# Performance work log

Hardware: AMD Instinct MI355X
Metric: run time of the kernel (lower is better)

Reference implementation:

```python
import jax, jax.numpy as jnp
import numpy as np


def _conv1x1(x, w, b):
    # x:[B,C,H,W], w:[O,C,1,1], b:[O]
    y = jax.lax.conv_general_dilated(x, w, (1, 1), 'SAME',
                                     dimension_numbers=('NCHW', 'OIHW', 'NCHW'))
    return y + b[None, :, None, None]


def _dwconv3x3(x, w, b):
    # depthwise: x:[B,C,H,W2], w:[C,1,3,3], b:[C]
    c = x.shape[1]
    y = jax.lax.conv_general_dilated(x, w, (1, 1), 'SAME',
                                     dimension_numbers=('NCHW', 'OIHW', 'NCHW'),
                                     feature_group_count=c)
    return y + b[None, :, None, None]


def setup_inputs() -> dict:
    key = jax.random.key(0)
    k1, k2, k3, k4, k5 = jax.random.split(key, 5)
    B, C, H, W = 4, 64, 256, 256
    x = jax.random.normal(k1, (B, C, H, W), dtype=jnp.float32)
    # qkv 1x1 conv params: [3C, C, 1, 1]
    w_qkv = jax.random.normal(k2, (3 * C, C, 1, 1), dtype=jnp.float32) * (1.0 / np.sqrt(C))
    b_qkv = jax.random.normal(k3, (3 * C,), dtype=jnp.float32) * 0.01
    # depthwise 3x3 conv params: [C, 1, 3, 3]
    w_dw = jax.random.normal(k4, (C, 1, 3, 3), dtype=jnp.float32) * (1.0 / 3.0)
    b_dw = jax.random.normal(k5, (C,), dtype=jnp.float32) * 0.01
    return {"x": x, "w_qkv": w_qkv, "b_qkv": b_qkv, "w_dw": w_dw, "b_dw": b_dw}


def reference(x, w_qkv, b_qkv, w_dw, b_dw):
    # qkv projection and split into q, k, v  (each [B,C,H,W])
    qkv = _conv1x1(x, w_qkv, b_qkv)
    q, k, v = jnp.split(qkv, 3, axis=1)
    # per-channel spatial attention scores: q @ k^T over last dim -> [B,C,H,H]
    scores = jnp.einsum('bchw,bcgw->bchg', q, k)
    # depthwise 3x3 conv on the [H,H] score map, then softmax over last dim
    attn = jax.nn.softmax(_dwconv3x3(scores, w_dw, b_dw), axis=-1)
    # attn @ v + residual -> [B,C,H,W]
    return jnp.einsum('bchg,bcgw->bchw', attn, v) + x
```

## Files before the change

### kernel.cpp

```cpp
#include <hip/hip_runtime.h>
#include <math.h>

#define B 4
#define C 64
#define H 256
#define W 256
#define HW (H*W)
#define CHW (C*HW)
#define BCHW (B*CHW)

typedef _Float16 half8v __attribute__((ext_vector_type(8)));
typedef float f32x4 __attribute__((ext_vector_type(4)));


__device__ inline ushort f16_bits(float f) {
    _Float16 h = (_Float16)f;
    return *(ushort*)&h;
}

__global__ __launch_bounds__(256, 4) void qkv_kernel(
    const float* __restrict__ x, const float* __restrict__ w,
    const float* __restrict__ bias, ushort* __restrict__ qkv)
{
    __shared__ ushort tile[48 * 264];
    int t = threadIdx.x;
    int lane = t & 63, wv = t >> 6;
    int l15 = lane & 15, l4 = lane >> 4;
    int p0 = blockIdx.x * 256;
    int b = p0 >> 16;
    int ppx = p0 & (HW - 1);
    int pxw = ppx + wv * 64;

    const float* xb = x + (size_t)b * CHW;

    half8v bfr[4][2];
    #pragma unroll
    for (int pf = 0; pf < 4; ++pf)
        #pragma unroll
        for (int kc = 0; kc < 2; ++kc) {
            int k0 = kc * 32 + l4 * 8;
            int px = pxw + pf * 16 + l15;
            half8v hv;
            #pragma unroll
            for (int j = 0; j < 8; ++j)
                hv[j] = (_Float16)xb[(size_t)(k0 + j) * HW + px];
            bfr[pf][kc] = hv;
        }

    #pragma unroll 1
    for (int ch = 0; ch < 4; ++ch) {
        int ocb = ch * 48;

        half8v afr[3][2];
        #pragma unroll
        for (int nf = 0; nf < 3; ++nf)
            #pragma unroll
            for (int kc = 0; kc < 2; ++kc) {
                int oc = ocb + nf * 16 + l15;
                int k0 = kc * 32 + l4 * 8;
                const float4* wp = (const float4*)&w[oc * 64 + k0];
                float4 wa = wp[0], wb = wp[1];
                half8v a;
                a[0] = (_Float16)wa.x; a[1] = (_Float16)wa.y;
                a[2] = (_Float16)wa.z; a[3] = (_Float16)wa.w;
                a[4] = (_Float16)wb.x; a[5] = (_Float16)wb.y;
                a[6] = (_Float16)wb.z; a[7] = (_Float16)wb.w;
                afr[nf][kc] = a;
            }

        f32x4 acc[3][4];
        #pragma unroll
        for (int nf = 0; nf < 3; ++nf)
            #pragma unroll
            for (int pf = 0; pf < 4; ++pf) acc[nf][pf] = (f32x4)0.f;

        #pragma unroll
        for (int kc = 0; kc < 2; ++kc)
            #pragma unroll
            for (int nf = 0; nf < 3; ++nf)
                #pragma unroll
                for (int pf = 0; pf < 4; ++pf)
                    acc[nf][pf] = __builtin_amdgcn_mfma_f32_16x16x32_f16(
                        afr[nf][kc], bfr[pf][kc], acc[nf][pf], 0, 0, 0);

        __syncthreads();
        #pragma unroll
        for (int nf = 0; nf < 3; ++nf)
            #pragma unroll
            for (int r = 0; r < 4; ++r) {
                int ocl = nf * 16 + l4 * 4 + r;
                float bv = bias[ocb + ocl];
                #pragma unroll
                for (int pf = 0; pf < 4; ++pf)
                    tile[ocl * 264 + wv * 64 + pf * 16 + l15] =
                        f16_bits(acc[nf][pf][r] + bv);
            }
        __syncthreads();

        #pragma unroll
        for (int j = 0; j < 6; ++j) {
            int id = t + 256 * j;
            int row = id >> 5, seg = id & 31;
            uint4 val = *(const uint4*)&tile[row * 264 + seg * 8];
            int oc = ocb + row;
            ushort* dst = qkv + (size_t)(oc >> 6) * BCHW
                        + ((size_t)b * 64 + (oc & 63)) * HW + ppx + seg * 8;
            *(uint4*)dst = val;
        }
    }
}

#define SST 266
#define YST 268
#define ATS 264
#define SOT 264
#define VSTR 268

__global__ __launch_bounds__(512, 2) void fused_kernel(
    const ushort* __restrict__ qf, const ushort* __restrict__ kf,
    const ushort* __restrict__ vf,
    const float* __restrict__ wdw, const float* __restrict__ bdw,
    const float* __restrict__ x, float* __restrict__ out)
{
    __shared__ float sbuf[34 * SST];
    __shared__ ushort qlds[48 * 256];
    __shared__ float mxf[32];

    int t = threadIdx.x;
    int lane = t & 63, wv = t >> 6;
    int l15 = lane & 15, l4 = lane >> 4;
    int col = t & 255, half = t >> 8;
    int base = half * 16;

    int bc = blockIdx.x;
    int c = bc & 63;

    const ushort* qb = qf + (size_t)bc * HW;
    const ushort* kb = kf + (size_t)bc * HW;
    const ushort* vb = vf + (size_t)bc * HW;
    const float*  xb = x  + (size_t)bc * HW;
    float*        ob = out + (size_t)bc * HW;

    int g0 = wv * 32;

    half8v ka[2][8];
    {
        const ushort* kr0 = kb + (g0 + l15) * 256 + l4 * 8;
        const ushort* kr1 = kb + (g0 + 16 + l15) * 256 + l4 * 8;
        #pragma unroll
        for (int kc = 0; kc < 8; ++kc) {
            ka[0][kc] = *(const half8v*)(kr0 + kc * 32);
            ka[1][kc] = *(const half8v*)(kr1 + kc * 32);
        }
    }

    half8v va[2][8];
    {
        ushort* vstage = (ushort*)sbuf;
        #pragma unroll
        for (int hc = 0; hc < 4; ++hc) {
            #pragma unroll
            for (int s = 0; s < 4; ++s) {
                int id = t + s * 512;
                int row = id >> 5, seg = id & 31;
                *(uint4*)&vstage[row * VSTR + seg * 8] =
                    *(const uint4*)(vb + (hc * 64 + row) * 256 + seg * 8);
            }
            __syncthreads();
            #pragma unroll
            for (int gf = 0; gf < 2; ++gf)
                #pragma unroll
                for (int kcl = 0; kcl < 2; ++kcl) {
                    half8v v;
                    #pragma unroll
                    for (int j = 0; j < 8; ++j)
                        v[j] = *(const _Float16*)&vstage[(kcl * 32 + l4 * 8 + j) * VSTR
                                                         + g0 + gf * 16 + l15];
                    va[gf][hc * 2 + kcl] = v;
                }
            __syncthreads();
        }
    }

    float w00 = wdw[c*9+0], w01 = wdw[c*9+1], w02 = wdw[c*9+2];
    float w10 = wdw[c*9+3], w11 = wdw[c*9+4], w12 = wdw[c*9+5];
    float w20 = wdw[c*9+6], w21 = wdw[c*9+7], w22 = wdw[c*9+8];
    float bias = bdw[c];

    half8v ones;
    #pragma unroll
    for (int j = 0; j < 8; ++j) ones[j] = (_Float16)1.0f;

    #pragma unroll 1
    for (int tile = 0; tile < 8; ++tile) {
        int h0 = tile * 32;

        #pragma unroll
        for (int s = 0; s < 3; ++s) {
            int id = t + s * 512;
            int row = id >> 5, cch = id & 31;
            int hq = min(max(h0 - 1 + row, 0), 255);
            uint4 val = *(const uint4*)(qb + hq * 256 + cch * 8);
            *(uint4*)((char*)qlds + row * 512 + ((cch ^ (row & 7)) << 4)) = val;
        }
        __syncthreads();

        {
            f32x4 acc[3][2];
            #pragma unroll
            for (int i = 0; i < 3; ++i)
                #pragma unroll
                for (int j = 0; j < 2; ++j) acc[i][j] = (f32x4)0.f;

            #pragma unroll
            for (int kc = 0; kc < 8; ++kc) {
                int ch4 = kc * 4 + l4;
                half8v q0 = *(const half8v*)((char*)qlds + (l15)      * 512 + ((ch4 ^ ( l15       & 7)) << 4));
                half8v q1 = *(const half8v*)((char*)qlds + (16 + l15) * 512 + ((ch4 ^ ((16 + l15) & 7)) << 4));
                half8v q2 = *(const half8v*)((char*)qlds + (32 + l15) * 512 + ((ch4 ^ ((32 + l15) & 7)) << 4));
                __builtin_amdgcn_s_setprio(1);
                acc[0][0] = __builtin_amdgcn_mfma_f32_16x16x32_f16(q0, ka[0][kc], acc[0][0], 0, 0, 0);
                acc[0][1] = __builtin_amdgcn_mfma_f32_16x16x32_f16(q0, ka[1][kc], acc[0][1], 0, 0, 0);
                acc[1][0] = __builtin_amdgcn_mfma_f32_16x16x32_f16(q1, ka[0][kc], acc[1][0], 0, 0, 0);
                acc[1][1] = __builtin_amdgcn_mfma_f32_16x16x32_f16(q1, ka[1][kc], acc[1][1], 0, 0, 0);
                acc[2][0] = __builtin_amdgcn_mfma_f32_16x16x32_f16(q2, ka[0][kc], acc[2][0], 0, 0, 0);
                acc[2][1] = __builtin_amdgcn_mfma_f32_16x16x32_f16(q2, ka[1][kc], acc[2][1], 0, 0, 0);
                __builtin_amdgcn_s_setprio(0);
            }
            #pragma unroll
            for (int hf = 0; hf < 3; ++hf)
                #pragma unroll
                for (int gf = 0; gf < 2; ++gf)
                    #pragma unroll
                    for (int r = 0; r < 4; ++r) {
                        int cr = hf * 16 + l4 * 4 + r;
                        if (cr < 34)
                            sbuf[cr * SST + g0 + gf * 16 + l15] = acc[hf][gf][r];
                    }
        }
        __syncthreads();

        float y[16];
        {
            float l0, m0, r0, l1, m1, r1;
            if (base == 0 && h0 == 0) { l0 = m0 = r0 = 0.f; }
            else {
                m0 = sbuf[base * SST + col];
                l0 = (col > 0)   ? sbuf[base * SST + col - 1] : 0.f;
                r0 = (col < 255) ? sbuf[base * SST + col + 1] : 0.f;
            }
            m1 = sbuf[(base + 1) * SST + col];
            l1 = (col > 0)   ? sbuf[(base + 1) * SST + col - 1] : 0.f;
            r1 = (col < 255) ? sbuf[(base + 1) * SST + col + 1] : 0.f;

            #pragma unroll
            for (int i = 0; i < 16; ++i) {
                float l2, m2, r2;
                if (h0 + base + i + 1 < 256) {
                    int sl = (base + i + 2) * SST;
                    m2 = sbuf[sl + col];
                    l2 = (col > 0)   ? sbuf[sl + col - 1] : 0.f;
                    r2 = (col < 255) ? sbuf[sl + col + 1] : 0.f;
                } else { l2 = m2 = r2 = 0.f; }
                y[i] = bias
                     + w00*l0 + w01*m0 + w02*r0
                     + w10*l1 + w11*m1 + w12*r1
                     + w20*l2 + w21*m2 + w22*r2;
                l0 = l1; m0 = m1; r0 = r1;
                l1 = l2; m1 = m2; r1 = r2;
            }
        }
        __syncthreads();

        float* yL = sbuf;
        #pragma unroll
        for (int i = 0; i < 16; ++i)
            yL[(base + i) * YST + col] = y[i];
        __syncthreads();

        {
            int r = t >> 4, c16 = t & 15;
            const f32x4* p = (const f32x4*)&yL[r * YST + c16 * 16];
            f32x4 v0 = p[0], v1 = p[1], v2 = p[2], v3 = p[3];
            float m = v0[0];
            #pragma unroll
            for (int j = 1; j < 4; ++j) m = fmaxf(m, v0[j]);
            #pragma unroll
            for (int j = 0; j < 4; ++j) m = fmaxf(m, v1[j]);
            #pragma unroll
            for (int j = 0; j < 4; ++j) m = fmaxf(m, v2[j]);
            #pragma unroll
            for (int j = 0; j < 4; ++j) m = fmaxf(m, v3[j]);
            m = fmaxf(m, __shfl_xor(m, 1));
            m = fmaxf(m, __shfl_xor(m, 2));
            m = fmaxf(m, __shfl_xor(m, 4));
            m = fmaxf(m, __shfl_xor(m, 8));
            if (c16 == 0) mxf[r] = m;
        }
        __syncthreads();

        ushort* attnb = (ushort*)sbuf;
        #pragma unroll
        for (int i = 0; i < 16; ++i) {
            float e = __expf(y[i] - mxf[base + i]);
            attnb[(base + i) * ATS + col] = f16_bits(e);
        }
        __syncthreads();

        f32x4 pacc[2][2], accs[2];
        #pragma unroll
        for (int i = 0; i < 2; ++i) {
            accs[i] = (f32x4)0.f;
            #pragma unroll
            for (int j = 0; j < 2; ++j) pacc[i][j] = (f32x4)0.f;
        }

        #pragma unroll
        for (int kc = 0; kc < 8; ++kc) {
            half8v af0 = *(const half8v*)&attnb[l15 * ATS + kc * 32 + l4 * 8];
            half8v af1 = *(const half8v*)&attnb[(16 + l15) * ATS + kc * 32 + l4 * 8];
            __builtin_amdgcn_s_setprio(1);
            pacc[0][0] = __builtin_amdgcn_mfma_f32_16x16x32_f16(af0, va[0][kc], pacc[0][0], 0, 0, 0);
            pacc[0][1] = __builtin_amdgcn_mfma_f32_16x16x32_f16(af0, va[1][kc], pacc[0][1], 0, 0, 0);
            accs[0]    = __builtin_amdgcn_mfma_f32_16x16x32_f16(af0, ones, accs[0], 0, 0, 0);
            pacc[1][0] = __builtin_amdgcn_mfma_f32_16x16x32_f16(af1, va[0][kc], pacc[1][0], 0, 0, 0);
            pacc[1][1] = __builtin_amdgcn_mfma_f32_16x16x32_f16(af1, va[1][kc], pacc[1][1], 0, 0, 0);
            accs[1]    = __builtin_amdgcn_mfma_f32_16x16x32_f16(af1, ones, accs[1], 0, 0, 0);
            __builtin_amdgcn_s_setprio(0);
        }
        __syncthreads();

        float* og = sbuf;
        #pragma unroll
        for (int hf = 0; hf < 2; ++hf)
            #pragma unroll
            for (int r = 0; r < 4; ++r) {
                int row = hf * 16 + l4 * 4 + r;
                float inv = 1.0f / accs[hf][r];
                #pragma unroll
                for (int wf = 0; wf < 2; ++wf)
                    og[row * SOT + g0 + wf * 16 + l15] = pacc[hf][wf][r] * inv;
            }
        __syncthreads();

        #pragma unroll
        for (int s = 0; s < 4; ++s) {
            int id = t + s * 512;
            int row = id >> 6, seg = id & 63;
            f32x4 v = *(const f32x4*)&og[row * SOT + seg * 4];
            f32x4 xr = *(const f32x4*)&xb[(h0 + row) * 256 + seg * 4];
            v += xr;
            *(f32x4*)&ob[(h0 + row) * 256 + seg * 4] = v;
        }
    }
}

extern "C" void kernel_launch(void* const* d_in, const int* in_sizes, int n_in,
                              void* d_out, int out_size, void* d_ws, size_t ws_size,
                              hipStream_t stream)
{
    const float* x     = (const float*)d_in[0];
    const float* w_qkv = (const float*)d_in[1];
    const float* b_qkv = (const float*)d_in[2];
    const float* w_dw  = (const float*)d_in[3];
    const float* b_dw  = (const float*)d_in[4];

    ushort* qf = (ushort*)d_ws;
    ushort* kf = qf + (size_t)BCHW;
    ushort* vf = kf + (size_t)BCHW;
    float*  out = (float*)d_out;

    qkv_kernel  <<<B * HW / 256, 256, 0, stream>>>(x, w_qkv, b_qkv, qf);
    fused_kernel<<<B * C,        512, 0, stream>>>(qf, kf, vf, w_dw, b_dw, x, out);
}
```

Measured before the change: 118.8 us.

## Prefetch next Q tile into registers and write output directly from accumulators

The Q rows for the next tile are now loaded from global memory into registers while the current tile's score and softmax phases run, then stored to LDS after the stencil phase. This hides global load latency behind compute and drops one LDS staging step at the top of each tile. The epilogue also drops the LDS round trip and two barriers. It writes attn·V plus the residual straight from the MFMA accumulators to global memory, at the cost of narrower, less coalesced scalar stores and loads of x and out, plus extra registers for the prefetch.

```diff
diff --git a/kernel.cpp b/kernel.cpp
--- a/kernel.cpp
+++ b/kernel.cpp
@@ -113,7 +113,6 @@
 #define SST 266
 #define YST 268
 #define ATS 264
-#define SOT 264
 #define VSTR 268
 
 __global__ __launch_bounds__(512, 2) void fused_kernel(
@@ -191,53 +190,75 @@
     #pragma unroll
     for (int j = 0; j < 8; ++j) ones[j] = (_Float16)1.0f;
 
+    int srow[3], scch[3];
+    #pragma unroll
+    for (int s = 0; s < 3; ++s) {
+        int id = t + s * 512;
+        srow[s] = id >> 5; scch[s] = id & 31;
+    }
+    uint4 sv0, sv1, sv2;
+
+    {
+        int hq0 = min(max(-1 + srow[0], 0), 255);
+        int hq1 = min(max(-1 + srow[1], 0), 255);
+        int hq2 = min(max(-1 + srow[2], 0), 255);
+        sv0 = *(const uint4*)(qb + hq0 * 256 + scch[0] * 8);
+        sv1 = *(const uint4*)(qb + hq1 * 256 + scch[1] * 8);
+        sv2 = *(const uint4*)(qb + hq2 * 256 + scch[2] * 8);
+        *(uint4*)((char*)qlds + srow[0] * 512 + ((scch[0] ^ (srow[0] & 7)) << 4)) = sv0;
+        *(uint4*)((char*)qlds + srow[1] * 512 + ((scch[1] ^ (srow[1] & 7)) << 4)) = sv1;
+        *(uint4*)((char*)qlds + srow[2] * 512 + ((scch[2] ^ (srow[2] & 7)) << 4)) = sv2;
+    }
+    __syncthreads();
+
     #pragma unroll 1
     for (int tile = 0; tile < 8; ++tile) {
         int h0 = tile * 32;
 
-        #pragma unroll
-        for (int s = 0; s < 3; ++s) {
-            int id = t + s * 512;
-            int row = id >> 5, cch = id & 31;
-            int hq = min(max(h0 - 1 + row, 0), 255);
-            uint4 val = *(const uint4*)(qb + hq * 256 + cch * 8);
-            *(uint4*)((char*)qlds + row * 512 + ((cch ^ (row & 7)) << 4)) = val;
-        }
+        f32x4 acc[3][2];
+        #pragma unroll
+        for (int i = 0; i < 3; ++i)
+            #pragma unroll
+            for (int j = 0; j < 2; ++j) acc[i][j] = (f32x4)0.f;
+
+        #pragma unroll
+        for (int kc = 0; kc < 8; ++kc) {
+            int ch4 = kc * 4 + l4;
+            half8v q0 = *(const half8v*)((char*)qlds + (l15)      * 512 + ((ch4 ^ ( l15       & 7)) << 4));
+            half8v q1 = *(const half8v*)((char*)qlds + (16 + l15) * 512 + ((ch4 ^ ((16 + l15) & 7)) << 4));
+            half8v q2 = *(const half8v*)((char*)qlds + (32 + l15) * 512 + ((ch4 ^ ((32 + l15) & 7)) << 4));
+            __builtin_amdgcn_s_setprio(1);
+            acc[0][0] = __builtin_amdgcn_mfma_f32_16x16x32_f16(q0, ka[0][kc], acc[0][0], 0, 0, 0);
+            acc[0][1] = __builtin_amdgcn_mfma_f32_16x16x32_f16(q0, ka[1][kc], acc[0][1], 0, 0, 0);
+            acc[1][0] = __builtin_amdgcn_mfma_f32_16x16x32_f16(q1, ka[0][kc], acc[1][0], 0, 0, 0);
+            acc[1][1] = __builtin_amdgcn_mfma_f32_16x16x32_f16(q1, ka[1][kc], acc[1][1], 0, 0, 0);
+            acc[2][0] = __builtin_amdgcn_mfma_f32_16x16x32_f16(q2, ka[0][kc], acc[2][0], 0, 0, 0);
+            acc[2][1] = __builtin_amdgcn_mfma_f32_16x16x32_f16(q2, ka[1][kc], acc[2][1], 0, 0, 0);
+            __builtin_amdgcn_s_setprio(0);
+        }
+
         __syncthreads();
 
         {
-            f32x4 acc[3][2];
-            #pragma unroll
-            for (int i = 0; i < 3; ++i)
-                #pragma unroll
-                for (int j = 0; j < 2; ++j) acc[i][j] = (f32x4)0.f;
-
-            #pragma unroll
-            for (int kc = 0; kc < 8; ++kc) {
-                int ch4 = kc * 4 + l4;
-                half8v q0 = *(const half8v*)((char*)qlds + (l15)      * 512 + ((ch4 ^ ( l15       & 7)) << 4));
-                half8v q1 = *(const half8v*)((char*)qlds + (16 + l15) * 512 + ((ch4 ^ ((16 + l15) & 7)) << 4));
-                half8v q2 = *(const half8v*)((char*)qlds + (32 + l15) * 512 + ((ch4 ^ ((32 + l15) & 7)) << 4));
-                __builtin_amdgcn_s_setprio(1);
-                acc[0][0] = __builtin_amdgcn_mfma_f32_16x16x32_f16(q0, ka[0][kc], acc[0][0], 0, 0, 0);
-                acc[0][1] = __builtin_amdgcn_mfma_f32_16x16x32_f16(q0, ka[1][kc], acc[0][1], 0, 0, 0);
-                acc[1][0] = __builtin_amdgcn_mfma_f32_16x16x32_f16(q1, ka[0][kc], acc[1][0], 0, 0, 0);
-                acc[1][1] = __builtin_amdgcn_mfma_f32_16x16x32_f16(q1, ka[1][kc], acc[1][1], 0, 0, 0);
-                acc[2][0] = __builtin_amdgcn_mfma_f32_16x16x32_f16(q2, ka[0][kc], acc[2][0], 0, 0, 0);
-                acc[2][1] = __builtin_amdgcn_mfma_f32_16x16x32_f16(q2, ka[1][kc], acc[2][1], 0, 0, 0);
-                __builtin_amdgcn_s_setprio(0);
-            }
-            #pragma unroll
-            for (int hf = 0; hf < 3; ++hf)
-                #pragma unroll
-                for (int gf = 0; gf < 2; ++gf)
-                    #pragma unroll
-                    for (int r = 0; r < 4; ++r) {
-                        int cr = hf * 16 + l4 * 4 + r;
-                        if (cr < 34)
-                            sbuf[cr * SST + g0 + gf * 16 + l15] = acc[hf][gf][r];
-                    }
-        }
+            int nh0 = h0 + 32;
+            int hq0 = min(max(nh0 - 1 + srow[0], 0), 255);
+            int hq1 = min(max(nh0 - 1 + srow[1], 0), 255);
+            int hq2 = min(max(nh0 - 1 + srow[2], 0), 255);
+            sv0 = *(const uint4*)(qb + hq0 * 256 + scch[0] * 8);
+            sv1 = *(const uint4*)(qb + hq1 * 256 + scch[1] * 8);
+            sv2 = *(const uint4*)(qb + hq2 * 256 + scch[2] * 8);
+        }
+
+        #pragma unroll
+        for (int hf = 0; hf < 3; ++hf)
+            #pragma unroll
+            for (int gf = 0; gf < 2; ++gf)
+                #pragma unroll
+                for (int r = 0; r < 4; ++r) {
+                    int cr = hf * 16 + l4 * 4 + r;
+                    if (cr < 34)
+                        sbuf[cr * SST + g0 + gf * 16 + l15] = acc[hf][gf][r];
+                }
         __syncthreads();
 
         float y[16];
@@ -272,6 +293,10 @@
         }
         __syncthreads();
 
+        *(uint4*)((char*)qlds + srow[0] * 512 + ((scch[0] ^ (srow[0] & 7)) << 4)) = sv0;
+        *(uint4*)((char*)qlds + srow[1] * 512 + ((scch[1] ^ (srow[1] & 7)) << 4)) = sv1;
+        *(uint4*)((char*)qlds + srow[2] * 512 + ((scch[2] ^ (srow[2] & 7)) << 4)) = sv2;
+
         float* yL = sbuf;
         #pragma unroll
         for (int i = 0; i < 16; ++i)
@@ -328,30 +353,20 @@
             accs[1]    = __builtin_amdgcn_mfma_f32_16x16x32_f16(af1, ones, accs[1], 0, 0, 0);
             __builtin_amdgcn_s_setprio(0);
         }
-        __syncthreads();
-
-        float* og = sbuf;
+
         #pragma unroll
         for (int hf = 0; hf < 2; ++hf)
             #pragma unroll
             for (int r = 0; r < 4; ++r) {
                 int row = hf * 16 + l4 * 4 + r;
                 float inv = 1.0f / accs[hf][r];
-                #pragma unroll
-                for (int wf = 0; wf < 2; ++wf)
-                    og[row * SOT + g0 + wf * 16 + l15] = pacc[hf][wf][r] * inv;
-            }
-        __syncthreads();
-
-        #pragma unroll
-        for (int s = 0; s < 4; ++s) {
-            int id = t + s * 512;
-            int row = id >> 6, seg = id & 63;
-            f32x4 v = *(const f32x4*)&og[row * SOT + seg * 4];
-            f32x4 xr = *(const f32x4*)&xb[(h0 + row) * 256 + seg * 4];
-            v += xr;
-            *(f32x4*)&ob[(h0 + row) * 256 + seg * 4] = v;
-        }
+                int hg = h0 + row;
+                #pragma unroll
+                for (int wf = 0; wf < 2; ++wf) {
+                    int wc = g0 + wf * 16 + l15;
+                    ob[hg * 256 + wc] = pacc[hf][wf][r] * inv + xb[hg * 256 + wc];
+                }
+            }
     }
 }
 
```

After: 153.8 us. 29.5% more time.
